# Optimization experiments

Hardware: AMD Instinct MI355X
Metric: run time of the kernel (lower is better)

## Reference

```python
import jax, jax.numpy as jnp
import numpy as np

B, L, D_IN, D_H, N_CLS = 512, 256, 300, 96, 20
N = B * L            # total nodes = 131072
DEG = 8
E = N * DEG          # 1,048,576 edges
VOCAB = 50001        # num_words + 1 (padding row)
STEP = 2
NEG_SLOPE = 0.2


def setup_inputs() -> dict:
    key = jax.random.key(0)
    ks = jax.random.split(key, 24)
    node_ids = jax.random.randint(ks[0], (N,), 0, 50000)
    # block-local edges: each edge stays within its graph's node range
    gid = jnp.repeat(jnp.arange(B), L * DEG)           # [E]
    src = gid * L + jax.random.randint(ks[1], (E,), 0, L)
    dst = gid * L + jax.random.randint(ks[2], (E,), 0, L)

    def xavier(k, shape):
        fan_in, fan_out = shape[0], shape[-1]
        a = float(np.sqrt(6.0 / (fan_in + fan_out)))
        return jax.random.uniform(k, shape, jnp.float32, -a, a)

    inp = {
        "node_ids": node_ids, "src": src, "dst": dst,
        "embed": jax.random.normal(ks[3], (VOCAB, D_IN), jnp.float32),
        "We": xavier(ks[4], (D_IN, D_H)), "be": jnp.zeros((D_H,), jnp.float32),
        "Wg": xavier(ks[5], (D_H, D_H)),
        "att_src": xavier(ks[6], (D_H,)), "att_dst": xavier(ks[7], (D_H,)),
        "bg": jnp.zeros((D_H,), jnp.float32),
        "Wz0": xavier(ks[8], (D_H, D_H)), "bz0": jnp.zeros((D_H,), jnp.float32),
        "Wz1": xavier(ks[9], (D_H, D_H)), "bz1": jnp.zeros((D_H,), jnp.float32),
        "Wr0": xavier(ks[10], (D_H, D_H)), "br0": jnp.zeros((D_H,), jnp.float32),
        "Wr1": xavier(ks[11], (D_H, D_H)), "br1": jnp.zeros((D_H,), jnp.float32),
        "Wh0": xavier(ks[12], (D_H, D_H)), "bh0": jnp.zeros((D_H,), jnp.float32),
        "Wh1": xavier(ks[13], (D_H, D_H)), "bh1": jnp.zeros((D_H,), jnp.float32),
        "Wemb": xavier(ks[14], (D_H, D_H)),
        "Wmlp": xavier(ks[15], (D_H, N_CLS)),
    }
    return inp


def _forward(node_ids, src, dst, embed, We, be, Wg, att_src, att_dst, bg,
             Wz0, bz0, Wz1, bz1, Wr0, br0, Wr1, br1, Wh0, bh0, Wh1, bh1,
             Wemb, Wmlp):
    # embedding lookup + encode (dropout off, eval)
    x = embed[node_ids]                                  # [N, D_IN]
    x = jnp.tanh(x @ We + be)                            # [N, D_H]

    # self loops (GATConv add_self_loops=True, heads=1)
    loop = jnp.arange(N)
    s = jnp.concatenate([src, loop])
    d = jnp.concatenate([dst, loop])

    for _ in range(STEP):
        # ---- GATConv ----
        h = x @ Wg                                       # [N, D_H]
        a_s = h @ att_src                                # [N]
        a_d = h @ att_dst                                # [N]
        e = a_s[s] + a_d[d]
        e = jnp.where(e > 0, e, NEG_SLOPE * e)           # leaky_relu
        # segment softmax over incoming edges of each target node
        m = jax.ops.segment_max(e, d, num_segments=N)
        ex = jnp.exp(e - m[d])
        denom = jax.ops.segment_sum(ex, d, num_segments=N)
        alpha = ex / denom[d]                            # [E+N]
        a = jax.ops.segment_sum(alpha[:, None] * h[s], d, num_segments=N) + bg
        # ---- GRU update (act=tanh) ----
        z = jax.nn.sigmoid(a @ Wz0 + bz0 + x @ Wz1 + bz1)
        r = jax.nn.sigmoid(a @ Wr0 + br0 + x @ Wr1 + br1)
        hh = jnp.tanh(a @ Wh0 + bh0 + (x * r) @ Wh1 + bh1)
        x = hh * z + x * (1.0 - z)

    # graph2batch: equal-length graphs -> reshape, mask is all ones
    xb = x.reshape(B, L, D_H)
    y = jnp.tanh(xb @ Wemb)                              # [B, L, D_H]
    pooled = y.max(axis=1) + y.mean(axis=1)              # max + mean readout
    return pooled @ Wmlp                                 # [B, N_CLS]


def reference(node_ids, src, dst, embed, We, be, Wg, att_src, att_dst, bg,
              Wz0, bz0, Wz1, bz1, Wr0, br0, Wr1, br1, Wh0, bh0, Wh1, bh1,
              Wemb, Wmlp):
    return _forward(node_ids, src, dst, embed, We, be, Wg, att_src, att_dst, bg,
                    Wz0, bz0, Wz1, bz1, Wr0, br0, Wr1, br1, Wh0, bh0, Wh1, bh1,
                    Wemb, Wmlp)
```

## Files before the change

### kernel.cpp

```cpp
#include <hip/hip_runtime.h>
#include <hip/hip_bf16.h>

#define NNODES 131072
#define LGRAPH 256
#define BGRAPH 512
#define DIN 300
#define DH 96
#define EPG 2048
#define VOCAB 50001
#define NCLS 20
#define NEG 0.2f
#define EMB_ROWS 50048
#define EMB_K 320
#define WS 100
#define XS 104

typedef __attribute__((ext_vector_type(4))) float f32x4;
typedef __attribute__((ext_vector_type(8))) short bf16x8;
typedef __attribute__((ext_vector_type(8))) unsigned short u16x8;
#define MFMA16(a, b, c) __builtin_amdgcn_mfma_f32_16x16x32_bf16(a, b, c, 0, 0, 0)

__device__ __forceinline__ unsigned short f2b(float f) {
  __hip_bfloat16 h = __float2bfloat16(f);
  return *reinterpret_cast<unsigned short*>(&h);
}
__device__ __forceinline__ float b2f(unsigned short u) {
  unsigned v = ((unsigned)u) << 16;
  return __uint_as_float(v);
}
__device__ __forceinline__ float sigm(float v) { return 1.f / (1.f + __expf(-v)); }
__device__ __forceinline__ float ftanh(float x) {
  float ax = fabsf(x);
  float e = __expf(ax + ax);
  float t = 1.f - 2.f / (e + 1.f);
  return copysignf(t, x);
}

__global__ void k_prep_w(const float* __restrict__ Wg, const float* __restrict__ Wz0,
                         const float* __restrict__ Wz1, const float* __restrict__ Wr0,
                         const float* __restrict__ Wr1, const float* __restrict__ Wh0,
                         const float* __restrict__ Wh1, const float* __restrict__ Wemb,
                         const float* __restrict__ We,
                         const float* __restrict__ bz0, const float* __restrict__ bz1,
                         const float* __restrict__ br0, const float* __restrict__ br1,
                         const float* __restrict__ bh0, const float* __restrict__ bh1,
                         unsigned short* __restrict__ WT, unsigned short* __restrict__ WeT,
                         float* __restrict__ bc) {
  const int b = blockIdx.x, t = threadIdx.x;
  if (b < 8) {
    const float* src = (b == 0) ? Wg : (b == 1) ? Wz0 : (b == 2) ? Wz1 : (b == 3) ? Wr0
                     : (b == 4) ? Wr1 : (b == 5) ? Wh0 : (b == 6) ? Wh1 : Wemb;
    unsigned short* dst = WT + b * DH * DH;
    for (int i = t; i < DH * DH; i += 256) {
      int c = i / DH, k = i - c * DH;
      dst[i] = f2b(src[k * DH + c]);
    }
  } else if (b == 8) {
    for (int i = t; i < DH * EMB_K; i += 256) {
      int c = i / EMB_K, k = i - c * EMB_K;
      WeT[i] = (k < DIN) ? f2b(We[k * DH + c]) : (unsigned short)0;
    }
  } else {
    if (t < DH) {
      bc[t] = bz0[t] + bz1[t];
      bc[DH + t] = br0[t] + br1[t];
      bc[2 * DH + t] = bh0[t] + bh1[t];
    }
  }
}

__device__ __forceinline__ bf16x8 ldcvt(const float* __restrict__ p, int row, int ko) {
  bf16x8 r;
  if (row < VOCAB) {
    float4 c0 = (ko + 4 <= DIN) ? *(const float4*)&p[row * DIN + ko]
                                : make_float4(0.f, 0.f, 0.f, 0.f);
    float4 c1 = (ko + 8 <= DIN) ? *(const float4*)&p[row * DIN + ko + 4]
                                : make_float4(0.f, 0.f, 0.f, 0.f);
    r[0] = (short)f2b(c0.x); r[1] = (short)f2b(c0.y);
    r[2] = (short)f2b(c0.z); r[3] = (short)f2b(c0.w);
    r[4] = (short)f2b(c1.x); r[5] = (short)f2b(c1.y);
    r[6] = (short)f2b(c1.z); r[7] = (short)f2b(c1.w);
  } else {
    #pragma unroll
    for (int j = 0; j < 8; ++j) r[j] = 0;
  }
  return r;
}

__global__ void k_emb_mm(const float* __restrict__ embed,
                         const unsigned short* __restrict__ WeT,
                         unsigned short* __restrict__ Tb) {
  const int t = threadIdx.x, w = t >> 6, l = t & 63, li = l & 15, lh = l >> 4;
  const int wbase = blockIdx.x * 128 + w * 32;
  f32x4 acc[2][6];
  #pragma unroll
  for (int rt = 0; rt < 2; rt++)
    #pragma unroll
    for (int ct = 0; ct < 6; ct++) acc[rt][ct] = (f32x4)0.f;
  for (int ks = 0; ks < 10; ++ks) {
    const int ko = lh * 8 + ks * 32;
    bf16x8 aA0 = ldcvt(embed, wbase + li, ko);
    bf16x8 aA1 = ldcvt(embed, wbase + 16 + li, ko);
    #pragma unroll
    for (int ct = 0; ct < 6; ct++) {
      bf16x8 bB = *(const bf16x8*)&WeT[(ct * 16 + li) * EMB_K + ko];
      acc[0][ct] = MFMA16(aA0, bB, acc[0][ct]);
      acc[1][ct] = MFMA16(aA1, bB, acc[1][ct]);
    }
  }
  #pragma unroll
  for (int rt = 0; rt < 2; rt++)
    #pragma unroll
    for (int ct = 0; ct < 6; ct++)
      #pragma unroll
      for (int r = 0; r < 4; r++)
        Tb[(wbase + rt * 16 + lh * 4 + r) * DH + ct * 16 + li] = f2b(acc[rt][ct][r]);
}

__global__ void k_gather(const int* __restrict__ ids, const unsigned short* __restrict__ Tb,
                         const float* __restrict__ be, unsigned short* __restrict__ xb) {
  const int total = NNODES * (DH / 8);
  for (int i = blockIdx.x * blockDim.x + threadIdx.x; i < total;
       i += gridDim.x * blockDim.x) {
    int n = i / (DH / 8);
    int q = i - n * (DH / 8);
    u16x8 v = *(const u16x8*)&Tb[ids[n] * DH + q * 8];
    u16x8 o;
    #pragma unroll
    for (int j = 0; j < 8; ++j) o[j] = f2b(ftanh(b2f(v[j]) + be[q * 8 + j]));
    *(u16x8*)&xb[i * 8] = o;
  }
}

__global__ __launch_bounds__(256) void k_h(
    const unsigned short* __restrict__ xb, const unsigned short* __restrict__ WgT,
    const float* __restrict__ att_s, const float* __restrict__ att_d,
    unsigned short* __restrict__ h, float* __restrict__ a_s,
    float* __restrict__ a_d) {
  __shared__ __align__(16) unsigned short sW[DH * WS];
  const int t = threadIdx.x, w = t >> 6, l = t & 63, li = l & 15, lh = l >> 4;
  const int wbase = blockIdx.x * 128 + w * 32;
  for (int i = t; i < DH * 12; i += 256) {
    int r = i / 12, c8 = i - r * 12;
    *(int4*)&sW[r * WS + c8 * 8] = *(const int4*)&WgT[r * DH + c8 * 8];
  }
  __syncthreads();
  f32x4 acc[2][6];
  #pragma unroll
  for (int rt = 0; rt < 2; rt++)
    #pragma unroll
    for (int ct = 0; ct < 6; ct++) acc[rt][ct] = (f32x4)0.f;
  #pragma unroll
  for (int ks = 0; ks < 3; ++ks) {
    const int ko = lh * 8 + ks * 32;
    bf16x8 aA0 = *(const bf16x8*)&xb[(wbase + li) * DH + ko];
    bf16x8 aA1 = *(const bf16x8*)&xb[(wbase + 16 + li) * DH + ko];
    #pragma unroll
    for (int ct = 0; ct < 6; ct++) {
      bf16x8 bB = *(const bf16x8*)&sW[(ct * 16 + li) * WS + ko];
      acc[0][ct] = MFMA16(aA0, bB, acc[0][ct]);
      acc[1][ct] = MFMA16(aA1, bB, acc[1][ct]);
    }
  }
  float ps[2][4] = {}, pd[2][4] = {};
  #pragma unroll
  for (int rt = 0; rt < 2; rt++)
    #pragma unroll
    for (int ct = 0; ct < 6; ct++) {
      const int col = ct * 16 + li;
      const float as_ = att_s[col], ad_ = att_d[col];
      #pragma unroll
      for (int r = 0; r < 4; r++) {
        float v = acc[rt][ct][r];
        h[(wbase + rt * 16 + lh * 4 + r) * DH + col] = f2b(v);
        ps[rt][r] += v * as_;
        pd[rt][r] += v * ad_;
      }
    }
  #pragma unroll
  for (int rt = 0; rt < 2; rt++)
    #pragma unroll
    for (int r = 0; r < 4; r++) {
      float s = ps[rt][r], d = pd[rt][r];
      #pragma unroll
      for (int m = 1; m < 16; m <<= 1) { s += __shfl_xor(s, m); d += __shfl_xor(d, m); }
      if (li == 0) {
        const int row = wbase + rt * 16 + lh * 4 + r;
        a_s[row] = s;
        a_d[row] = d;
      }
    }
}

__global__ __launch_bounds__(512, 4) void k_att(
    const int* __restrict__ src, const int* __restrict__ dst,
    const unsigned short* __restrict__ h, const float* __restrict__ a_sg,
    const float* __restrict__ a_dg, const float* __restrict__ bg,
    unsigned short* __restrict__ aout) {
  __shared__ __align__(16) unsigned short sH[LGRAPH * XS];
  __shared__ float s_ev[EPG];
  __shared__ unsigned char s_sl[EPG], s_dl[EPG];
  __shared__ unsigned char s_srcS[EPG];
  __shared__ int s_cnt[LGRAPH], s_off[LGRAPH], s_pos[LGRAPH];
  __shared__ float s_as[LGRAPH], s_ad[LGRAPH];
  __shared__ float s_bg[DH];
  const int g = blockIdx.x, t = threadIdx.x;
  const int nb = g * LGRAPH;
  if (t < LGRAPH) { s_cnt[t] = 0; s_as[t] = a_sg[nb + t]; s_ad[t] = a_dg[nb + t]; }
  if (t < DH) s_bg[t] = bg[t];
  #pragma unroll
  for (int j = 0; j < 6; ++j) {
    int idx = t + 512 * j;
    int row = idx / 12, ch = idx - row * 12;
    *(int4*)&sH[row * XS + ch * 8] = *(const int4*)&h[(nb + row) * DH + ch * 8];
  }
  __syncthreads();
  for (int e = t; e < EPG; e += 512) {
    int sl = src[g * EPG + e] - nb, dl = dst[g * EPG + e] - nb;
    s_sl[e] = (unsigned char)sl;
    s_dl[e] = (unsigned char)dl;
    atomicAdd(&s_cnt[dl], 1);
  }
  __syncthreads();
  if (t < 64) {
    int carry = 0;
    #pragma unroll
    for (int c = 0; c < 4; ++c) {
      int v = s_cnt[c * 64 + t];
      int x = v;
      #pragma unroll
      for (int o = 1; o < 64; o <<= 1) {
        int y = __shfl_up(x, o);
        if (t >= o) x += y;
      }
      s_off[c * 64 + t] = x - v + carry;
      carry += __shfl(x, 63);
    }
  }
  __syncthreads();
  if (t < LGRAPH) s_pos[t] = s_off[t];
  __syncthreads();
  for (int e = t; e < EPG; e += 512) {
    int sl = s_sl[e], dl = s_dl[e];
    float ee = s_as[sl] + s_ad[dl];
    ee = ee > 0.f ? ee : NEG * ee;
    int pos = atomicAdd(&s_pos[dl], 1);
    s_srcS[pos] = (unsigned char)sl;
    s_ev[pos] = ee;
  }
  __syncthreads();
  {
    const int d = t >> 1, half = t & 1;
    const int beg = s_off[d], end = beg + s_cnt[d];
    float ss = s_as[d] + s_ad[d];
    ss = ss > 0.f ? ss : NEG * ss;
    float m = ss;
    for (int i = beg; i < end; ++i) m = fmaxf(m, s_ev[i]);
    const int cbase = half * 48;
    float acc[48];
    float wself = __expf(ss - m);
    float den = wself;
    #pragma unroll
    for (int k = 0; k < 6; ++k) {
      u16x8 v = *(const u16x8*)&sH[d * XS + cbase + k * 8];
      #pragma unroll
      for (int j = 0; j < 8; ++j) acc[k * 8 + j] = wself * b2f(v[j]);
    }
    for (int i = beg; i < end; ++i) {
      float wv = __expf(s_ev[i] - m);
      den += wv;
      int sl2 = s_srcS[i];
      #pragma unroll
      for (int k = 0; k < 6; ++k) {
        u16x8 v = *(const u16x8*)&sH[sl2 * XS + cbase + k * 8];
        #pragma unroll
        for (int j = 0; j < 8; ++j) acc[k * 8 + j] += wv * b2f(v[j]);
      }
    }
    float inv = 1.f / den;
    unsigned short* op = &aout[(nb + d) * DH + cbase];
    #pragma unroll
    for (int k = 0; k < 6; ++k) {
      u16x8 o;
      #pragma unroll
      for (int j = 0; j < 8; ++j) o[j] = f2b(acc[k * 8 + j] * inv + s_bg[cbase + k * 8 + j]);
      *(u16x8*)&op[k * 8] = o;
    }
  }
}

__global__ __launch_bounds__(512, 2) void k_gru(
    const unsigned short* __restrict__ ab, unsigned short* __restrict__ xb,
    const unsigned short* __restrict__ WT, const float* __restrict__ bc) {
  __shared__ __align__(16) unsigned short sW[6 * DH * WS];
  __shared__ __align__(16) unsigned short sX[128 * WS];
  const int t = threadIdx.x, w = t >> 6, l = t & 63, li = l & 15, lh = l >> 4;
  const int wr = w >> 1, wc = w & 1;
  #pragma unroll
  for (int m = 0; m < 6; ++m) {
    const int srcm = (m == 0) ? 3 : (m == 1) ? 4 : (m == 2) ? 1 : (m == 3) ? 2 : (m == 4) ? 5 : 6;
    const unsigned short* srcp = WT + srcm * DH * DH;
    for (int i = t; i < DH * 12; i += 512) {
      int r = i / 12, c8 = i - r * 12;
      *(int4*)&sW[(m * DH + r) * WS + c8 * 8] = *(const int4*)&srcp[r * DH + c8 * 8];
    }
  }
  float zb_[3], rb_[3], hb_[3];
  #pragma unroll
  for (int ct = 0; ct < 3; ++ct) {
    const int col = wc * 48 + ct * 16 + li;
    zb_[ct] = bc[col]; rb_[ct] = bc[DH + col]; hb_[ct] = bc[2 * DH + col];
  }

  for (int tile = 0; tile < 4; ++tile) {
    const int nb0 = (blockIdx.x * 4 + tile) * 128;
    __syncthreads();
    #pragma unroll
    for (int j = 0; j < 3; ++j) {
      int idx = t + 512 * j;
      int row = idx / 12, ch = idx - row * 12;
      *(int4*)&sX[row * WS + ch * 8] = *(const int4*)&xb[(nb0 + row) * DH + ch * 8];
    }
    __syncthreads();
    bf16x8 aA[2][3], aX[2][3];
    #pragma unroll
    for (int rt = 0; rt < 2; rt++)
      #pragma unroll
      for (int ks = 0; ks < 3; ks++) {
        const int row = wr * 32 + rt * 16 + li;
        const int ko = lh * 8 + ks * 32;
        aA[rt][ks] = *(const bf16x8*)&ab[(nb0 + row) * DH + ko];
        aX[rt][ks] = *(const bf16x8*)&sX[row * WS + ko];
      }
    float xo[2][3][4];
    #pragma unroll
    for (int rt = 0; rt < 2; rt++)
      #pragma unroll
      for (int ct = 0; ct < 3; ct++)
        #pragma unroll
        for (int r = 0; r < 4; r++)
          xo[rt][ct][r] = b2f(sX[(wr * 32 + rt * 16 + lh * 4 + r) * WS + wc * 48 + ct * 16 + li]);
    f32x4 accR[2][3], accZ[2][3];
    #pragma unroll
    for (int rt = 0; rt < 2; rt++)
      #pragma unroll
      for (int ct = 0; ct < 3; ct++) { accR[rt][ct] = (f32x4)0.f; accZ[rt][ct] = (f32x4)0.f; }
    #pragma unroll
    for (int ks = 0; ks < 3; ks++) {
      const int ko = lh * 8 + ks * 32;
      #pragma unroll
      for (int ct = 0; ct < 3; ct++) {
        const int wrow = wc * 48 + ct * 16 + li;
        bf16x8 w_r0 = *(const bf16x8*)&sW[(0 * DH + wrow) * WS + ko];
        bf16x8 w_r1 = *(const bf16x8*)&sW[(1 * DH + wrow) * WS + ko];
        bf16x8 w_z0 = *(const bf16x8*)&sW[(2 * DH + wrow) * WS + ko];
        bf16x8 w_z1 = *(const bf16x8*)&sW[(3 * DH + wrow) * WS + ko];
        #pragma unroll
        for (int rt = 0; rt < 2; rt++) {
          accR[rt][ct] = MFMA16(aA[rt][ks], w_r0, accR[rt][ct]);
          accR[rt][ct] = MFMA16(aX[rt][ks], w_r1, accR[rt][ct]);
          accZ[rt][ct] = MFMA16(aA[rt][ks], w_z0, accZ[rt][ct]);
          accZ[rt][ct] = MFMA16(aX[rt][ks], w_z1, accZ[rt][ct]);
        }
      }
    }
    __syncthreads();
    #pragma unroll
    for (int rt = 0; rt < 2; rt++)
      #pragma unroll
      for (int ct = 0; ct < 3; ct++) {
        const int col = wc * 48 + ct * 16 + li;
        #pragma unroll
        for (int r = 0; r < 4; r++) {
          float rv = sigm(accR[rt][ct][r] + rb_[ct]);
          sX[(wr * 32 + rt * 16 + lh * 4 + r) * WS + col] = f2b(xo[rt][ct][r] * rv);
        }
      }
    __syncthreads();
    bf16x8 aU[2][3];
    #pragma unroll
    for (int rt = 0; rt < 2; rt++)
      #pragma unroll
      for (int ks = 0; ks < 3; ks++)
        aU[rt][ks] = *(const bf16x8*)&sX[(wr * 32 + rt * 16 + li) * WS + lh * 8 + ks * 32];
    __syncthreads();
    f32x4 accH[2][3];
    #pragma unroll
    for (int rt = 0; rt < 2; rt++)
      #pragma unroll
      for (int ct = 0; ct < 3; ct++) accH[rt][ct] = (f32x4)0.f;
    #pragma unroll
    for (int ks = 0; ks < 3; ks++) {
      const int ko = lh * 8 + ks * 32;
      #pragma unroll
      for (int ct = 0; ct < 3; ct++) {
        const int wrow = wc * 48 + ct * 16 + li;
        bf16x8 w_h0 = *(const bf16x8*)&sW[(4 * DH + wrow) * WS + ko];
        bf16x8 w_h1 = *(const bf16x8*)&sW[(5 * DH + wrow) * WS + ko];
        #pragma unroll
        for (int rt = 0; rt < 2; rt++) {
          accH[rt][ct] = MFMA16(aA[rt][ks], w_h0, accH[rt][ct]);
          accH[rt][ct] = MFMA16(aU[rt][ks], w_h1, accH[rt][ct]);
        }
      }
    }
    #pragma unroll
    for (int rt = 0; rt < 2; rt++)
      #pragma unroll
      for (int ct = 0; ct < 3; ct++) {
        const int col = wc * 48 + ct * 16 + li;
        #pragma unroll
        for (int r = 0; r < 4; r++) {
          float z = sigm(accZ[rt][ct][r] + zb_[ct]);
          float hh = ftanh(accH[rt][ct][r] + hb_[ct]);
          float xn = hh * z + xo[rt][ct][r] * (1.f - z);
          sX[(wr * 32 + rt * 16 + lh * 4 + r) * WS + col] = f2b(xn);
        }
      }
    __syncthreads();
    #pragma unroll
    for (int j = 0; j < 3; ++j) {
      int idx = t + 512 * j;
      int row = idx / 12, ch = idx - row * 12;
      *(int4*)&xb[(nb0 + row) * DH + ch * 8] = *(const int4*)&sX[row * WS + ch * 8];
    }
  }
}

__global__ __launch_bounds__(256) void k_readout(
    const unsigned short* __restrict__ xb, const unsigned short* __restrict__ WembT,
    const float* __restrict__ Wmlp, float* __restrict__ out) {
  __shared__ __align__(16) unsigned short sW[DH * WS];
  __shared__ float pmaxs[4][DH], psums[4][DH];
  __shared__ float spool[DH];
  const int g = blockIdx.x, t = threadIdx.x, w = t >> 6, l = t & 63, li = l & 15, lh = l >> 4;
  const int wbase = g * LGRAPH + w * 64;
  for (int i = t; i < DH * 12; i += 256) {
    int r = i / 12, c8 = i - r * 12;
    *(int4*)&sW[r * WS + c8 * 8] = *(const int4*)&WembT[r * DH + c8 * 8];
  }
  __syncthreads();
  f32x4 acc[4][6];
  #pragma unroll
  for (int rt = 0; rt < 4; rt++)
    #pragma unroll
    for (int ct = 0; ct < 6; ct++) acc[rt][ct] = (f32x4)0.f;
  #pragma unroll
  for (int ks = 0; ks < 3; ks++) {
    const int ko = lh * 8 + ks * 32;
    bf16x8 aA[4];
    #pragma unroll
    for (int rt = 0; rt < 4; rt++)
      aA[rt] = *(const bf16x8*)&xb[(wbase + rt * 16 + li) * DH + ko];
    #pragma unroll
    for (int ct = 0; ct < 6; ct++) {
      bf16x8 bB = *(const bf16x8*)&sW[(ct * 16 + li) * WS + ko];
      #pragma unroll
      for (int rt = 0; rt < 4; rt++) acc[rt][ct] = MFMA16(aA[rt], bB, acc[rt][ct]);
    }
  }
  float pm[6], psu[6];
  #pragma unroll
  for (int ct = 0; ct < 6; ct++) {
    float mx = -1e30f, sm = 0.f;
    #pragma unroll
    for (int rt = 0; rt < 4; rt++)
      #pragma unroll
      for (int r = 0; r < 4; r++) {
        float y = ftanh(acc[rt][ct][r]);
        mx = fmaxf(mx, y);
        sm += y;
      }
    pm[ct] = mx; psu[ct] = sm;
  }
  #pragma unroll
  for (int ct = 0; ct < 6; ct++) {
    pm[ct] = fmaxf(pm[ct], __shfl_xor(pm[ct], 16));
    psu[ct] += __shfl_xor(psu[ct], 16);
    pm[ct] = fmaxf(pm[ct], __shfl_xor(pm[ct], 32));
    psu[ct] += __shfl_xor(psu[ct], 32);
  }
  if (lh == 0) {
    #pragma unroll
    for (int ct = 0; ct < 6; ct++) {
      pmaxs[w][ct * 16 + li] = pm[ct];
      psums[w][ct * 16 + li] = psu[ct];
    }
  }
  __syncthreads();
  if (t < DH) {
    float mx = fmaxf(fmaxf(pmaxs[0][t], pmaxs[1][t]), fmaxf(pmaxs[2][t], pmaxs[3][t]));
    float sm = psums[0][t] + psums[1][t] + psums[2][t] + psums[3][t];
    spool[t] = mx + sm * (1.f / LGRAPH);
  }
  __syncthreads();
  if (t < NCLS) {
    float a = 0.f;
    for (int k = 0; k < DH; ++k) a += spool[k] * Wmlp[k * NCLS + t];
    out[g * NCLS + t] = a;
  }
}

extern "C" void kernel_launch(void* const* d_in, const int* in_sizes, int n_in,
                              void* d_out, int out_size, void* d_ws, size_t ws_size,
                              hipStream_t stream) {
  const int*   node_ids = (const int*)d_in[0];
  const int*   src      = (const int*)d_in[1];
  const int*   dst      = (const int*)d_in[2];
  const float* embed    = (const float*)d_in[3];
  const float* We   = (const float*)d_in[4];
  const float* be   = (const float*)d_in[5];
  const float* Wg   = (const float*)d_in[6];
  const float* att_src = (const float*)d_in[7];
  const float* att_dst = (const float*)d_in[8];
  const float* bg   = (const float*)d_in[9];
  const float* Wz0  = (const float*)d_in[10];
  const float* bz0  = (const float*)d_in[11];
  const float* Wz1  = (const float*)d_in[12];
  const float* bz1  = (const float*)d_in[13];
  const float* Wr0  = (const float*)d_in[14];
  const float* br0  = (const float*)d_in[15];
  const float* Wr1  = (const float*)d_in[16];
  const float* br1  = (const float*)d_in[17];
  const float* Wh0  = (const float*)d_in[18];
  const float* bh0  = (const float*)d_in[19];
  const float* Wh1  = (const float*)d_in[20];
  const float* bh1  = (const float*)d_in[21];
  const float* Wemb = (const float*)d_in[22];
  const float* Wmlp = (const float*)d_in[23];
  float* out = (float*)d_out;

  char* w_ = (char*)d_ws;
  unsigned short* xb   = (unsigned short*)(w_ + 0);
  unsigned short* ab   = (unsigned short*)(w_ + 25165824);
  unsigned short* h    = (unsigned short*)(w_ + 50331648);
  unsigned short* Tb   = (unsigned short*)(w_ + 75497472);
  float*          a_s  = (float*)(w_ + 85106688);
  float*          a_d  = (float*)(w_ + 85630976);
  unsigned short* WT   = (unsigned short*)(w_ + 86155264);
  unsigned short* WeT  = (unsigned short*)(w_ + 86302720);
  float*          bc   = (float*)(w_ + 86364160);

  unsigned short* WgT  = WT + 0 * DH * DH;
  unsigned short* WembT= WT + 7 * DH * DH;

  hipLaunchKernelGGL(k_prep_w, dim3(10), dim3(256), 0, stream,
                     Wg, Wz0, Wz1, Wr0, Wr1, Wh0, Wh1, Wemb, We,
                     bz0, bz1, br0, br1, bh0, bh1, WT, WeT, bc);
  hipLaunchKernelGGL(k_emb_mm, dim3(EMB_ROWS / 128), dim3(256), 0, stream, embed, WeT, Tb);
  hipLaunchKernelGGL(k_gather, dim3(2048), dim3(256), 0, stream, node_ids, Tb, be, xb);
  for (int s = 0; s < 2; ++s) {
    hipLaunchKernelGGL(k_h, dim3(NNODES / 128), dim3(256), 0, stream,
                       xb, WgT, att_src, att_dst, h, a_s, a_d);
    hipLaunchKernelGGL(k_att, dim3(BGRAPH), dim3(512), 0, stream,
                       src, dst, h, a_s, a_d, bg, ab);
    hipLaunchKernelGGL(k_gru, dim3(256), dim3(512), 0, stream, ab, xb, WT, bc);
  }
  hipLaunchKernelGGL(k_readout, dim3(BGRAPH), dim3(256), 0, stream, xb, WembT, Wmlp, out);
}
```

Measured before the change: 246.0 us.

## Fuse gather with GAT projection, GRU with next projection and readout

Merges the embedding gather and tanh into the first GAT linear kernel, fuses the GRU update of step one with the next step's Wg projection and attention logits, and fuses the final GRU with the Wemb projection, max+mean pooling and MLP. The aim is to cut kernel launches and avoid re-reading xb from global memory between stages. Weight fragments are now held in registers, which raises register pressure, and the fused GRU kernels add extra syncs and per-tile work.

```diff
diff --git a/kernel.cpp b/kernel.cpp
--- a/kernel.cpp
+++ b/kernel.cpp
@@ -117,51 +117,57 @@
         Tb[(wbase + rt * 16 + lh * 4 + r) * DH + ct * 16 + li] = f2b(acc[rt][ct][r]);
 }
 
-__global__ void k_gather(const int* __restrict__ ids, const unsigned short* __restrict__ Tb,
-                         const float* __restrict__ be, unsigned short* __restrict__ xb) {
-  const int total = NNODES * (DH / 8);
-  for (int i = blockIdx.x * blockDim.x + threadIdx.x; i < total;
-       i += gridDim.x * blockDim.x) {
-    int n = i / (DH / 8);
-    int q = i - n * (DH / 8);
-    u16x8 v = *(const u16x8*)&Tb[ids[n] * DH + q * 8];
+__global__ __launch_bounds__(256) void k_gh(
+    const int* __restrict__ ids, const unsigned short* __restrict__ Tb,
+    const float* __restrict__ be, const unsigned short* __restrict__ WgT,
+    const float* __restrict__ att_s, const float* __restrict__ att_d,
+    unsigned short* __restrict__ xb, unsigned short* __restrict__ h,
+    float* __restrict__ a_s, float* __restrict__ a_d) {
+  __shared__ __align__(16) unsigned short sX[128 * XS];
+  __shared__ int s_id[128];
+  __shared__ float s_be[DH];
+  const int t = threadIdx.x, w = t >> 6, l = t & 63, li = l & 15, lh = l >> 4;
+  const int nb0 = blockIdx.x * 128;
+  bf16x8 WF[6][3];
+  #pragma unroll
+  for (int ct = 0; ct < 6; ++ct)
+    #pragma unroll
+    for (int ks = 0; ks < 3; ++ks)
+      WF[ct][ks] = *(const bf16x8*)&WgT[(ct * 16 + li) * DH + lh * 8 + ks * 32];
+  if (t < 128) s_id[t] = ids[nb0 + t];
+  if (t < DH) s_be[t] = be[t];
+  __syncthreads();
+  #pragma unroll
+  for (int j = 0; j < 6; ++j) {
+    int idx = t + 256 * j;
+    int row = idx / 12, ch = idx - row * 12;
+    u16x8 v = *(const u16x8*)&Tb[s_id[row] * DH + ch * 8];
     u16x8 o;
     #pragma unroll
-    for (int j = 0; j < 8; ++j) o[j] = f2b(ftanh(b2f(v[j]) + be[q * 8 + j]));
-    *(u16x8*)&xb[i * 8] = o;
-  }
-}
-
-__global__ __launch_bounds__(256) void k_h(
-    const unsigned short* __restrict__ xb, const unsigned short* __restrict__ WgT,
-    const float* __restrict__ att_s, const float* __restrict__ att_d,
-    unsigned short* __restrict__ h, float* __restrict__ a_s,
-    float* __restrict__ a_d) {
-  __shared__ __align__(16) unsigned short sW[DH * WS];
-  const int t = threadIdx.x, w = t >> 6, l = t & 63, li = l & 15, lh = l >> 4;
-  const int wbase = blockIdx.x * 128 + w * 32;
-  for (int i = t; i < DH * 12; i += 256) {
-    int r = i / 12, c8 = i - r * 12;
-    *(int4*)&sW[r * WS + c8 * 8] = *(const int4*)&WgT[r * DH + c8 * 8];
+    for (int k = 0; k < 8; ++k) o[k] = f2b(ftanh(b2f(v[k]) + s_be[ch * 8 + k]));
+    *(u16x8*)&sX[row * XS + ch * 8] = o;
+    *(u16x8*)&xb[(nb0 + row) * DH + ch * 8] = o;
   }
   __syncthreads();
+  const int wbase = w * 32;
   f32x4 acc[2][6];
   #pragma unroll
   for (int rt = 0; rt < 2; rt++)
     #pragma unroll
     for (int ct = 0; ct < 6; ct++) acc[rt][ct] = (f32x4)0.f;
-  #pragma unroll
-  for (int ks = 0; ks < 3; ++ks) {
-    const int ko = lh * 8 + ks * 32;
-    bf16x8 aA0 = *(const bf16x8*)&xb[(wbase + li) * DH + ko];
-    bf16x8 aA1 = *(const bf16x8*)&xb[(wbase + 16 + li) * DH + ko];
+  bf16x8 aA[2][3];
+  #pragma unroll
+  for (int rt = 0; rt < 2; rt++)
+    #pragma unroll
+    for (int ks = 0; ks < 3; ks++)
+      aA[rt][ks] = *(const bf16x8*)&sX[(wbase + rt * 16 + li) * XS + lh * 8 + ks * 32];
+  #pragma unroll
+  for (int ks = 0; ks < 3; ++ks)
     #pragma unroll
     for (int ct = 0; ct < 6; ct++) {
-      bf16x8 bB = *(const bf16x8*)&sW[(ct * 16 + li) * WS + ko];
-      acc[0][ct] = MFMA16(aA0, bB, acc[0][ct]);
-      acc[1][ct] = MFMA16(aA1, bB, acc[1][ct]);
-    }
-  }
+      acc[0][ct] = MFMA16(aA[0][ks], WF[ct][ks], acc[0][ct]);
+      acc[1][ct] = MFMA16(aA[1][ks], WF[ct][ks], acc[1][ct]);
+    }
   float ps[2][4] = {}, pd[2][4] = {};
   #pragma unroll
   for (int rt = 0; rt < 2; rt++)
@@ -172,7 +178,7 @@
       #pragma unroll
       for (int r = 0; r < 4; r++) {
         float v = acc[rt][ct][r];
-        h[(wbase + rt * 16 + lh * 4 + r) * DH + col] = f2b(v);
+        h[(nb0 + wbase + rt * 16 + lh * 4 + r) * DH + col] = f2b(v);
         ps[rt][r] += v * as_;
         pd[rt][r] += v * ad_;
       }
@@ -185,7 +191,7 @@
       #pragma unroll
       for (int m = 1; m < 16; m <<= 1) { s += __shfl_xor(s, m); d += __shfl_xor(d, m); }
       if (li == 0) {
-        const int row = wbase + rt * 16 + lh * 4 + r;
+        const int row = nb0 + wbase + rt * 16 + lh * 4 + r;
         a_s[row] = s;
         a_d[row] = d;
       }
@@ -289,28 +295,140 @@
   }
 }
 
-__global__ __launch_bounds__(512, 2) void k_gru(
+#define GRU_TILE_BODY                                                          \
+    bf16x8 aA[2][3], aX[2][3];                                                 \
+    _Pragma("unroll")                                                          \
+    for (int rt = 0; rt < 2; rt++)                                             \
+      _Pragma("unroll")                                                        \
+      for (int ks = 0; ks < 3; ks++) {                                         \
+        const int row = wr * 32 + rt * 16 + li;                                \
+        const int ko = lh * 8 + ks * 32;                                       \
+        aA[rt][ks] = *(const bf16x8*)&ab[(nb0 + row) * DH + ko];               \
+        aX[rt][ks] = *(const bf16x8*)&sX[row * WS + ko];                       \
+      }                                                                        \
+    float xo[2][3][4];                                                         \
+    _Pragma("unroll")                                                          \
+    for (int rt = 0; rt < 2; rt++)                                             \
+      _Pragma("unroll")                                                        \
+      for (int ct = 0; ct < 3; ct++)                                           \
+        _Pragma("unroll")                                                      \
+        for (int r = 0; r < 4; r++)                                            \
+          xo[rt][ct][r] = b2f(sX[(wr * 32 + rt * 16 + lh * 4 + r) * WS + wc * 48 + ct * 16 + li]); \
+    f32x4 accR[2][3], accZ[2][3];                                              \
+    _Pragma("unroll")                                                          \
+    for (int rt = 0; rt < 2; rt++)                                             \
+      _Pragma("unroll")                                                        \
+      for (int ct = 0; ct < 3; ct++) { accR[rt][ct] = (f32x4)0.f; accZ[rt][ct] = (f32x4)0.f; } \
+    _Pragma("unroll")                                                          \
+    for (int ks = 0; ks < 3; ks++) {                                           \
+      const int ko = lh * 8 + ks * 32;                                         \
+      _Pragma("unroll")                                                        \
+      for (int ct = 0; ct < 3; ct++) {                                         \
+        const int wrow = wc * 48 + ct * 16 + li;                               \
+        bf16x8 w_r0 = *(const bf16x8*)&sW[(0 * DH + wrow) * WS + ko];          \
+        bf16x8 w_r1 = *(const bf16x8*)&sW[(1 * DH + wrow) * WS + ko];          \
+        bf16x8 w_z0 = *(const bf16x8*)&sW[(2 * DH + wrow) * WS + ko];          \
+        bf16x8 w_z1 = *(const bf16x8*)&sW[(3 * DH + wrow) * WS + ko];          \
+        _Pragma("unroll")                                                      \
+        for (int rt = 0; rt < 2; rt++) {                                       \
+          accR[rt][ct] = MFMA16(aA[rt][ks], w_r0, accR[rt][ct]);               \
+          accR[rt][ct] = MFMA16(aX[rt][ks], w_r1, accR[rt][ct]);               \
+          accZ[rt][ct] = MFMA16(aA[rt][ks], w_z0, accZ[rt][ct]);               \
+          accZ[rt][ct] = MFMA16(aX[rt][ks], w_z1, accZ[rt][ct]);               \
+        }                                                                      \
+      }                                                                        \
+    }                                                                          \
+    __syncthreads();                                                           \
+    _Pragma("unroll")                                                          \
+    for (int rt = 0; rt < 2; rt++)                                             \
+      _Pragma("unroll")                                                        \
+      for (int ct = 0; ct < 3; ct++) {                                         \
+        const int col = wc * 48 + ct * 16 + li;                                \
+        _Pragma("unroll")                                                      \
+        for (int r = 0; r < 4; r++) {                                          \
+          float rv = sigm(accR[rt][ct][r] + rb_[ct]);                          \
+          sX[(wr * 32 + rt * 16 + lh * 4 + r) * WS + col] = f2b(xo[rt][ct][r] * rv); \
+        }                                                                      \
+      }                                                                        \
+    __syncthreads();                                                           \
+    bf16x8 aU[2][3];                                                           \
+    _Pragma("unroll")                                                          \
+    for (int rt = 0; rt < 2; rt++)                                             \
+      _Pragma("unroll")                                                        \
+      for (int ks = 0; ks < 3; ks++)                                           \
+        aU[rt][ks] = *(const bf16x8*)&sX[(wr * 32 + rt * 16 + li) * WS + lh * 8 + ks * 32]; \
+    __syncthreads();                                                           \
+    f32x4 accH[2][3];                                                          \
+    _Pragma("unroll")                                                          \
+    for (int rt = 0; rt < 2; rt++)                                             \
+      _Pragma("unroll")                                                        \
+      for (int ct = 0; ct < 3; ct++) accH[rt][ct] = (f32x4)0.f;                \
+    _Pragma("unroll")                                                          \
+    for (int ks = 0; ks < 3; ks++) {                                           \
+      const int ko = lh * 8 + ks * 32;                                         \
+      _Pragma("unroll")                                                        \
+      for (int ct = 0; ct < 3; ct++) {                                         \
+        const int wrow = wc * 48 + ct * 16 + li;                               \
+        bf16x8 w_h0 = *(const bf16x8*)&sW[(4 * DH + wrow) * WS + ko];          \
+        bf16x8 w_h1 = *(const bf16x8*)&sW[(5 * DH + wrow) * WS + ko];          \
+        _Pragma("unroll")                                                      \
+        for (int rt = 0; rt < 2; rt++) {                                       \
+          accH[rt][ct] = MFMA16(aA[rt][ks], w_h0, accH[rt][ct]);               \
+          accH[rt][ct] = MFMA16(aU[rt][ks], w_h1, accH[rt][ct]);               \
+        }                                                                      \
+      }                                                                        \
+    }                                                                          \
+    _Pragma("unroll")                                                          \
+    for (int rt = 0; rt < 2; rt++)                                             \
+      _Pragma("unroll")                                                        \
+      for (int ct = 0; ct < 3; ct++) {                                         \
+        const int col = wc * 48 + ct * 16 + li;                                \
+        _Pragma("unroll")                                                      \
+        for (int r = 0; r < 4; r++) {                                          \
+          float z = sigm(accZ[rt][ct][r] + zb_[ct]);                           \
+          float hh = ftanh(accH[rt][ct][r] + hb_[ct]);                         \
+          float xn = hh * z + xo[rt][ct][r] * (1.f - z);                       \
+          sX[(wr * 32 + rt * 16 + lh * 4 + r) * WS + col] = f2b(xn);           \
+        }                                                                      \
+      }                                                                        \
+    __syncthreads();
+
+#define GRU_STAGE_W                                                            \
+  _Pragma("unroll")                                                            \
+  for (int m = 0; m < 6; ++m) {                                                \
+    const int srcm = (m == 0) ? 3 : (m == 1) ? 4 : (m == 2) ? 1 : (m == 3) ? 2 : (m == 4) ? 5 : 6; \
+    const unsigned short* srcp = WT + srcm * DH * DH;                          \
+    for (int i = t; i < DH * 12; i += 512) {                                   \
+      int r = i / 12, c8 = i - r * 12;                                         \
+      *(int4*)&sW[(m * DH + r) * WS + c8 * 8] = *(const int4*)&srcp[r * DH + c8 * 8]; \
+    }                                                                          \
+  }                                                                            \
+  float zb_[3], rb_[3], hb_[3];                                                \
+  _Pragma("unroll")                                                            \
+  for (int ct = 0; ct < 3; ++ct) {                                             \
+    const int col = wc * 48 + ct * 16 + li;                                    \
+    zb_[ct] = bc[col]; rb_[ct] = bc[DH + col]; hb_[ct] = bc[2 * DH + col];     \
+  }
+
+__global__ __launch_bounds__(512, 2) void k_gru_h(
     const unsigned short* __restrict__ ab, unsigned short* __restrict__ xb,
-    const unsigned short* __restrict__ WT, const float* __restrict__ bc) {
+    const unsigned short* __restrict__ WT, const float* __restrict__ bc,
+    const unsigned short* __restrict__ WgT,
+    const float* __restrict__ att_s, const float* __restrict__ att_d,
+    unsigned short* __restrict__ h, float* __restrict__ a_s,
+    float* __restrict__ a_d) {
   __shared__ __align__(16) unsigned short sW[6 * DH * WS];
   __shared__ __align__(16) unsigned short sX[128 * WS];
+  __shared__ float s_red[128][2][2];
   const int t = threadIdx.x, w = t >> 6, l = t & 63, li = l & 15, lh = l >> 4;
   const int wr = w >> 1, wc = w & 1;
-  #pragma unroll
-  for (int m = 0; m < 6; ++m) {
-    const int srcm = (m == 0) ? 3 : (m == 1) ? 4 : (m == 2) ? 1 : (m == 3) ? 2 : (m == 4) ? 5 : 6;
-    const unsigned short* srcp = WT + srcm * DH * DH;
-    for (int i = t; i < DH * 12; i += 512) {
-      int r = i / 12, c8 = i - r * 12;
-      *(int4*)&sW[(m * DH + r) * WS + c8 * 8] = *(const int4*)&srcp[r * DH + c8 * 8];
-    }
-  }
-  float zb_[3], rb_[3], hb_[3];
-  #pragma unroll
-  for (int ct = 0; ct < 3; ++ct) {
-    const int col = wc * 48 + ct * 16 + li;
-    zb_[ct] = bc[col]; rb_[ct] = bc[DH + col]; hb_[ct] = bc[2 * DH + col];
-  }
+  bf16x8 WF[3][3];
+  #pragma unroll
+  for (int ct = 0; ct < 3; ++ct)
+    #pragma unroll
+    for (int ks = 0; ks < 3; ++ks)
+      WF[ct][ks] = *(const bf16x8*)&WgT[(wc * 48 + ct * 16 + li) * DH + lh * 8 + ks * 32];
+  GRU_STAGE_W
 
   for (int tile = 0; tile < 4; ++tile) {
     const int nb0 = (blockIdx.x * 4 + tile) * 128;
@@ -322,182 +440,159 @@
       *(int4*)&sX[row * WS + ch * 8] = *(const int4*)&xb[(nb0 + row) * DH + ch * 8];
     }
     __syncthreads();
-    bf16x8 aA[2][3], aX[2][3];
-    #pragma unroll
-    for (int rt = 0; rt < 2; rt++)
-      #pragma unroll
-      for (int ks = 0; ks < 3; ks++) {
-        const int row = wr * 32 + rt * 16 + li;
-        const int ko = lh * 8 + ks * 32;
-        aA[rt][ks] = *(const bf16x8*)&ab[(nb0 + row) * DH + ko];
-        aX[rt][ks] = *(const bf16x8*)&sX[row * WS + ko];
-      }
-    float xo[2][3][4];
-    #pragma unroll
-    for (int rt = 0; rt < 2; rt++)
-      #pragma unroll
-      for (int ct = 0; ct < 3; ct++)
-        #pragma unroll
-        for (int r = 0; r < 4; r++)
-          xo[rt][ct][r] = b2f(sX[(wr * 32 + rt * 16 + lh * 4 + r) * WS + wc * 48 + ct * 16 + li]);
-    f32x4 accR[2][3], accZ[2][3];
-    #pragma unroll
-    for (int rt = 0; rt < 2; rt++)
-      #pragma unroll
-      for (int ct = 0; ct < 3; ct++) { accR[rt][ct] = (f32x4)0.f; accZ[rt][ct] = (f32x4)0.f; }
-    #pragma unroll
-    for (int ks = 0; ks < 3; ks++) {
-      const int ko = lh * 8 + ks * 32;
-      #pragma unroll
-      for (int ct = 0; ct < 3; ct++) {
-        const int wrow = wc * 48 + ct * 16 + li;
-        bf16x8 w_r0 = *(const bf16x8*)&sW[(0 * DH + wrow) * WS + ko];
-        bf16x8 w_r1 = *(const bf16x8*)&sW[(1 * DH + wrow) * WS + ko];
-        bf16x8 w_z0 = *(const bf16x8*)&sW[(2 * DH + wrow) * WS + ko];
-        bf16x8 w_z1 = *(const bf16x8*)&sW[(3 * DH + wrow) * WS + ko];
-        #pragma unroll
-        for (int rt = 0; rt < 2; rt++) {
-          accR[rt][ct] = MFMA16(aA[rt][ks], w_r0, accR[rt][ct]);
-          accR[rt][ct] = MFMA16(aX[rt][ks], w_r1, accR[rt][ct]);
-          accZ[rt][ct] = MFMA16(aA[rt][ks], w_z0, accZ[rt][ct]);
-          accZ[rt][ct] = MFMA16(aX[rt][ks], w_z1, accZ[rt][ct]);
-        }
-      }
-    }
-    __syncthreads();
-    #pragma unroll
-    for (int rt = 0; rt < 2; rt++)
-      #pragma unroll
-      for (int ct = 0; ct < 3; ct++) {
-        const int col = wc * 48 + ct * 16 + li;
-        #pragma unroll
-        for (int r = 0; r < 4; r++) {
-          float rv = sigm(accR[rt][ct][r] + rb_[ct]);
-          sX[(wr * 32 + rt * 16 + lh * 4 + r) * WS + col] = f2b(xo[rt][ct][r] * rv);
-        }
-      }
-    __syncthreads();
-    bf16x8 aU[2][3];
-    #pragma unroll
-    for (int rt = 0; rt < 2; rt++)
-      #pragma unroll
-      for (int ks = 0; ks < 3; ks++)
-        aU[rt][ks] = *(const bf16x8*)&sX[(wr * 32 + rt * 16 + li) * WS + lh * 8 + ks * 32];
-    __syncthreads();
-    f32x4 accH[2][3];
-    #pragma unroll
-    for (int rt = 0; rt < 2; rt++)
-      #pragma unroll
-      for (int ct = 0; ct < 3; ct++) accH[rt][ct] = (f32x4)0.f;
-    #pragma unroll
-    for (int ks = 0; ks < 3; ks++) {
-      const int ko = lh * 8 + ks * 32;
-      #pragma unroll
-      for (int ct = 0; ct < 3; ct++) {
-        const int wrow = wc * 48 + ct * 16 + li;
-        bf16x8 w_h0 = *(const bf16x8*)&sW[(4 * DH + wrow) * WS + ko];
-        bf16x8 w_h1 = *(const bf16x8*)&sW[(5 * DH + wrow) * WS + ko];
-        #pragma unroll
-        for (int rt = 0; rt < 2; rt++) {
-          accH[rt][ct] = MFMA16(aA[rt][ks], w_h0, accH[rt][ct]);
-          accH[rt][ct] = MFMA16(aU[rt][ks], w_h1, accH[rt][ct]);
-        }
-      }
-    }
-    #pragma unroll
-    for (int rt = 0; rt < 2; rt++)
-      #pragma unroll
-      for (int ct = 0; ct < 3; ct++) {
-        const int col = wc * 48 + ct * 16 + li;
-        #pragma unroll
-        for (int r = 0; r < 4; r++) {
-          float z = sigm(accZ[rt][ct][r] + zb_[ct]);
-          float hh = ftanh(accH[rt][ct][r] + hb_[ct]);
-          float xn = hh * z + xo[rt][ct][r] * (1.f - z);
-          sX[(wr * 32 + rt * 16 + lh * 4 + r) * WS + col] = f2b(xn);
-        }
-      }
-    __syncthreads();
+    GRU_TILE_BODY
     #pragma unroll
     for (int j = 0; j < 3; ++j) {
       int idx = t + 512 * j;
       int row = idx / 12, ch = idx - row * 12;
       *(int4*)&xb[(nb0 + row) * DH + ch * 8] = *(const int4*)&sX[row * WS + ch * 8];
     }
-  }
-}
-
-__global__ __launch_bounds__(256) void k_readout(
-    const unsigned short* __restrict__ xb, const unsigned short* __restrict__ WembT,
-    const float* __restrict__ Wmlp, float* __restrict__ out) {
-  __shared__ __align__(16) unsigned short sW[DH * WS];
-  __shared__ float pmaxs[4][DH], psums[4][DH];
+    bf16x8 aN[2][3];
+    #pragma unroll
+    for (int rt = 0; rt < 2; rt++)
+      #pragma unroll
+      for (int ks = 0; ks < 3; ks++)
+        aN[rt][ks] = *(const bf16x8*)&sX[(wr * 32 + rt * 16 + li) * WS + lh * 8 + ks * 32];
+    f32x4 accN[2][3];
+    #pragma unroll
+    for (int rt = 0; rt < 2; rt++)
+      #pragma unroll
+      for (int ct = 0; ct < 3; ct++) accN[rt][ct] = (f32x4)0.f;
+    #pragma unroll
+    for (int ks = 0; ks < 3; ks++)
+      #pragma unroll
+      for (int ct = 0; ct < 3; ct++) {
+        accN[0][ct] = MFMA16(aN[0][ks], WF[ct][ks], accN[0][ct]);
+        accN[1][ct] = MFMA16(aN[1][ks], WF[ct][ks], accN[1][ct]);
+      }
+    float ps[2][4] = {}, pd[2][4] = {};
+    #pragma unroll
+    for (int rt = 0; rt < 2; rt++)
+      #pragma unroll
+      for (int ct = 0; ct < 3; ct++) {
+        const int col = wc * 48 + ct * 16 + li;
+        const float as_ = att_s[col], ad_ = att_d[col];
+        #pragma unroll
+        for (int r = 0; r < 4; r++) {
+          float v = accN[rt][ct][r];
+          h[(nb0 + wr * 32 + rt * 16 + lh * 4 + r) * DH + col] = f2b(v);
+          ps[rt][r] += v * as_;
+          pd[rt][r] += v * ad_;
+        }
+      }
+    #pragma unroll
+    for (int rt = 0; rt < 2; rt++)
+      #pragma unroll
+      for (int r = 0; r < 4; r++) {
+        float s = ps[rt][r], d = pd[rt][r];
+        #pragma unroll
+        for (int m = 1; m < 16; m <<= 1) { s += __shfl_xor(s, m); d += __shfl_xor(d, m); }
+        if (li == 0) {
+          const int rl = wr * 32 + rt * 16 + lh * 4 + r;
+          s_red[rl][wc][0] = s;
+          s_red[rl][wc][1] = d;
+        }
+      }
+    __syncthreads();
+    if (t < 128) {
+      a_s[nb0 + t] = s_red[t][0][0] + s_red[t][1][0];
+      a_d[nb0 + t] = s_red[t][0][1] + s_red[t][1][1];
+    }
+  }
+}
+
+__global__ __launch_bounds__(512, 2) void k_gru_ro(
+    const unsigned short* __restrict__ ab, const unsigned short* __restrict__ xb,
+    const unsigned short* __restrict__ WT, const float* __restrict__ bc,
+    const unsigned short* __restrict__ WembT, const float* __restrict__ Wmlp,
+    float* __restrict__ out) {
+  __shared__ __align__(16) unsigned short sW[6 * DH * WS];
+  __shared__ __align__(16) unsigned short sX[128 * WS];
+  __shared__ float s_pm[4][DH], s_ps[4][DH];
   __shared__ float spool[DH];
-  const int g = blockIdx.x, t = threadIdx.x, w = t >> 6, l = t & 63, li = l & 15, lh = l >> 4;
-  const int wbase = g * LGRAPH + w * 64;
-  for (int i = t; i < DH * 12; i += 256) {
-    int r = i / 12, c8 = i - r * 12;
-    *(int4*)&sW[r * WS + c8 * 8] = *(const int4*)&WembT[r * DH + c8 * 8];
-  }
-  __syncthreads();
-  f32x4 acc[4][6];
-  #pragma unroll
-  for (int rt = 0; rt < 4; rt++)
-    #pragma unroll
-    for (int ct = 0; ct < 6; ct++) acc[rt][ct] = (f32x4)0.f;
-  #pragma unroll
-  for (int ks = 0; ks < 3; ks++) {
-    const int ko = lh * 8 + ks * 32;
-    bf16x8 aA[4];
-    #pragma unroll
-    for (int rt = 0; rt < 4; rt++)
-      aA[rt] = *(const bf16x8*)&xb[(wbase + rt * 16 + li) * DH + ko];
-    #pragma unroll
-    for (int ct = 0; ct < 6; ct++) {
-      bf16x8 bB = *(const bf16x8*)&sW[(ct * 16 + li) * WS + ko];
-      #pragma unroll
-      for (int rt = 0; rt < 4; rt++) acc[rt][ct] = MFMA16(aA[rt], bB, acc[rt][ct]);
-    }
-  }
-  float pm[6], psu[6];
-  #pragma unroll
-  for (int ct = 0; ct < 6; ct++) {
-    float mx = -1e30f, sm = 0.f;
-    #pragma unroll
-    for (int rt = 0; rt < 4; rt++)
-      #pragma unroll
-      for (int r = 0; r < 4; r++) {
-        float y = ftanh(acc[rt][ct][r]);
-        mx = fmaxf(mx, y);
-        sm += y;
-      }
-    pm[ct] = mx; psu[ct] = sm;
-  }
-  #pragma unroll
-  for (int ct = 0; ct < 6; ct++) {
-    pm[ct] = fmaxf(pm[ct], __shfl_xor(pm[ct], 16));
-    psu[ct] += __shfl_xor(psu[ct], 16);
-    pm[ct] = fmaxf(pm[ct], __shfl_xor(pm[ct], 32));
-    psu[ct] += __shfl_xor(psu[ct], 32);
-  }
-  if (lh == 0) {
-    #pragma unroll
-    for (int ct = 0; ct < 6; ct++) {
-      pmaxs[w][ct * 16 + li] = pm[ct];
-      psums[w][ct * 16 + li] = psu[ct];
-    }
-  }
-  __syncthreads();
-  if (t < DH) {
-    float mx = fmaxf(fmaxf(pmaxs[0][t], pmaxs[1][t]), fmaxf(pmaxs[2][t], pmaxs[3][t]));
-    float sm = psums[0][t] + psums[1][t] + psums[2][t] + psums[3][t];
-    spool[t] = mx + sm * (1.f / LGRAPH);
-  }
-  __syncthreads();
-  if (t < NCLS) {
-    float a = 0.f;
-    for (int k = 0; k < DH; ++k) a += spool[k] * Wmlp[k * NCLS + t];
-    out[g * NCLS + t] = a;
+  const int t = threadIdx.x, w = t >> 6, l = t & 63, li = l & 15, lh = l >> 4;
+  const int wr = w >> 1, wc = w & 1;
+  bf16x8 WF[3][3];
+  #pragma unroll
+  for (int ct = 0; ct < 3; ++ct)
+    #pragma unroll
+    for (int ks = 0; ks < 3; ++ks)
+      WF[ct][ks] = *(const bf16x8*)&WembT[(wc * 48 + ct * 16 + li) * DH + lh * 8 + ks * 32];
+  GRU_STAGE_W
+
+  float pmr[3], psr[3];
+  for (int tile = 0; tile < 4; ++tile) {
+    const int nb0 = (blockIdx.x * 4 + tile) * 128;
+    if ((tile & 1) == 0) {
+      #pragma unroll
+      for (int ct = 0; ct < 3; ++ct) { pmr[ct] = -1e30f; psr[ct] = 0.f; }
+    }
+    __syncthreads();
+    #pragma unroll
+    for (int j = 0; j < 3; ++j) {
+      int idx = t + 512 * j;
+      int row = idx / 12, ch = idx - row * 12;
+      *(int4*)&sX[row * WS + ch * 8] = *(const int4*)&xb[(nb0 + row) * DH + ch * 8];
+    }
+    __syncthreads();
+    GRU_TILE_BODY
+    bf16x8 aN[2][3];
+    #pragma unroll
+    for (int rt = 0; rt < 2; rt++)
+      #pragma unroll
+      for (int ks = 0; ks < 3; ks++)
+        aN[rt][ks] = *(const bf16x8*)&sX[(wr * 32 + rt * 16 + li) * WS + lh * 8 + ks * 32];
+    f32x4 accE[2][3];
+    #pragma unroll
+    for (int rt = 0; rt < 2; rt++)
+      #pragma unroll
+      for (int ct = 0; ct < 3; ct++) accE[rt][ct] = (f32x4)0.f;
+    #pragma unroll
+    for (int ks = 0; ks < 3; ks++)
+      #pragma unroll
+      for (int ct = 0; ct < 3; ct++) {
+        accE[0][ct] = MFMA16(aN[0][ks], WF[ct][ks], accE[0][ct]);
+        accE[1][ct] = MFMA16(aN[1][ks], WF[ct][ks], accE[1][ct]);
+      }
+    #pragma unroll
+    for (int ct = 0; ct < 3; ct++)
+      #pragma unroll
+      for (int rt = 0; rt < 2; rt++)
+        #pragma unroll
+        for (int r = 0; r < 4; r++) {
+          float y = ftanh(accE[rt][ct][r]);
+          pmr[ct] = fmaxf(pmr[ct], y);
+          psr[ct] += y;
+        }
+    if (tile & 1) {
+      #pragma unroll
+      for (int ct = 0; ct < 3; ct++) {
+        pmr[ct] = fmaxf(pmr[ct], __shfl_xor(pmr[ct], 16));
+        psr[ct] += __shfl_xor(psr[ct], 16);
+        pmr[ct] = fmaxf(pmr[ct], __shfl_xor(pmr[ct], 32));
+        psr[ct] += __shfl_xor(psr[ct], 32);
+      }
+      if (lh == 0) {
+        #pragma unroll
+        for (int ct = 0; ct < 3; ct++) {
+          s_pm[wr][wc * 48 + ct * 16 + li] = pmr[ct];
+          s_ps[wr][wc * 48 + ct * 16 + li] = psr[ct];
+        }
+      }
+      __syncthreads();
+      if (t < DH) {
+        float mx = fmaxf(fmaxf(s_pm[0][t], s_pm[1][t]), fmaxf(s_pm[2][t], s_pm[3][t]));
+        float sm = s_ps[0][t] + s_ps[1][t] + s_ps[2][t] + s_ps[3][t];
+        spool[t] = mx + sm * (1.f / LGRAPH);
+      }
+      __syncthreads();
+      if (t < NCLS) {
+        const int g = blockIdx.x * 2 + (tile >> 1);
+        float a = 0.f;
+        for (int k = 0; k < DH; ++k) a += spool[k] * Wmlp[k * NCLS + t];
+        out[g * NCLS + t] = a;
+      }
+    }
   }
 }
 
@@ -541,20 +636,21 @@
   unsigned short* WeT  = (unsigned short*)(w_ + 86302720);
   float*          bc   = (float*)(w_ + 86364160);
 
-  unsigned short* WgT  = WT + 0 * DH * DH;
-  unsigned short* WembT= WT + 7 * DH * DH;
+  unsigned short* WgT   = WT + 0 * DH * DH;
+  unsigned short* WembT = WT + 7 * DH * DH;
 
   hipLaunchKernelGGL(k_prep_w, dim3(10), dim3(256), 0, stream,
                      Wg, Wz0, Wz1, Wr0, Wr1, Wh0, Wh1, Wemb, We,
                      bz0, bz1, br0, br1, bh0, bh1, WT, WeT, bc);
   hipLaunchKernelGGL(k_emb_mm, dim3(EMB_ROWS / 128), dim3(256), 0, stream, embed, WeT, Tb);
-  hipLaunchKernelGGL(k_gather, dim3(2048), dim3(256), 0, stream, node_ids, Tb, be, xb);
-  for (int s = 0; s < 2; ++s) {
-    hipLaunchKernelGGL(k_h, dim3(NNODES / 128), dim3(256), 0, stream,
-                       xb, WgT, att_src, att_dst, h, a_s, a_d);
-    hipLaunchKernelGGL(k_att, dim3(BGRAPH), dim3(512), 0, stream,
-                       src, dst, h, a_s, a_d, bg, ab);
-    hipLaunchKernelGGL(k_gru, dim3(256), dim3(512), 0, stream, ab, xb, WT, bc);
-  }
-  hipLaunchKernelGGL(k_readout, dim3(BGRAPH), dim3(256), 0, stream, xb, WembT, Wmlp, out);
-}
+  hipLaunchKernelGGL(k_gh, dim3(NNODES / 128), dim3(256), 0, stream,
+                     node_ids, Tb, be, WgT, att_src, att_dst, xb, h, a_s, a_d);
+  hipLaunchKernelGGL(k_att, dim3(BGRAPH), dim3(512), 0, stream,
+                     src, dst, h, a_s, a_d, bg, ab);
+  hipLaunchKernelGGL(k_gru_h, dim3(256), dim3(512), 0, stream,
+                     ab, xb, WT, bc, WgT, att_src, att_dst, h, a_s, a_d);
+  hipLaunchKernelGGL(k_att, dim3(BGRAPH), dim3(512), 0, stream,
+                     src, dst, h, a_s, a_d, bg, ab);
+  hipLaunchKernelGGL(k_gru_ro, dim3(256), dim3(512), 0, stream,
+                     ab, xb, WT, bc, WembT, Wmlp, out);
+}
```

Measured after the change: 266.7 us. +8.4%, slower.
